# Performance work log

Measured on AMD Instinct MI355X. Metric: run time of the kernel, lower is better.

## Reference

```python
import jax, jax.numpy as jnp
import numpy as np

L = 3          # num_layer
D = 128        # emb_dim
N_INST = 40000
N_NET = 10000
N = N_INST + N_NET
E = 800000
EPS = 1e-5


def setup_inputs() -> dict:
    key = jax.random.key(0)
    ks = jax.random.split(key, 16)
    g = lambda k, shape: jax.random.normal(k, shape, jnp.float32) * 0.05
    return {
        'x': jax.random.normal(ks[0], (N_INST, 11), jnp.float32),
        'x_net': jax.random.normal(ks[1], (N_NET, 3), jnp.float32),
        # encoder for instance nodes: 11 -> 2D -> D
        'enc_W1': g(ks[2], (2 * D, 11)), 'enc_b1': jnp.zeros((2 * D,), jnp.float32),
        'enc_W2': g(ks[3], (D, 2 * D)), 'enc_b2': jnp.zeros((D,), jnp.float32),
        # encoder for net nodes: 3 -> D -> D
        'encn_W1': g(ks[4], (D, 3)), 'encn_b1': jnp.zeros((D,), jnp.float32),
        'encn_W2': g(ks[5], (D, D)), 'encn_b2': jnp.zeros((D,), jnp.float32),
        # forward-direction GCN convs
        'conv_W': g(ks[6], (L, D, D)), 'conv_b': jnp.zeros((L, D), jnp.float32),
        'conv_root': g(ks[7], (L, D)),
        # reverse-direction GCN convs
        'rconv_W': g(ks[8], (L, D, D)), 'rconv_b': jnp.zeros((L, D), jnp.float32),
        'rconv_root': g(ks[9], (L, D)),
        # layernorms
        'ln_g': jnp.ones((L, D), jnp.float32), 'ln_b': jnp.zeros((L, D), jnp.float32),
        # graph edge list
        'src': jax.random.randint(ks[10], (E,), 0, N, jnp.int32),
        'dst': jax.random.randint(ks[11], (E,), 0, N, jnp.int32),
        'num_instances': N_INST,
    }


def _lrelu(v):
    return jnp.where(v >= 0, v, 0.1 * v)


def _gcn_conv(h, W, b, root, e_src, e_dst, deg, dinv):
    # h: [N, D]; e_src/e_dst: [E]; deg/dinv: [N]
    x = h @ W.T + b                                   # [N, D]
    norm = dinv[e_src] * dinv[e_dst]                  # [E]
    msg = norm[:, None] * jax.nn.relu(x[e_src])       # [E, D] gather + scale
    agg = jax.ops.segment_sum(msg, e_dst, num_segments=N)  # [N, D] scatter-add
    self_loop = jax.nn.relu(x + root) / deg[:, None]
    return agg + self_loop


def reference(x, x_net, enc_W1, enc_b1, enc_W2, enc_b2,
              encn_W1, encn_b1, encn_W2, encn_b2,
              conv_W, conv_b, conv_root, rconv_W, rconv_b, rconv_root,
              ln_g, ln_b, src, dst, num_instances):
    # node encoders
    h_inst = _lrelu(_lrelu(x @ enc_W1.T + enc_b1) @ enc_W2.T + enc_b2)
    h_net = _lrelu(_lrelu(x_net @ encn_W1.T + encn_b1) @ encn_W2.T + encn_b2)
    h = jnp.concatenate([h_inst, h_net], axis=0)      # [N, D]

    ones = jnp.ones((E,), jnp.float32)
    deg_in = jax.ops.segment_sum(ones, dst, num_segments=N) + 1.0
    deg_out = jax.ops.segment_sum(ones, src, num_segments=N) + 1.0
    dinv_in = jnp.where(jnp.isinf(deg_in ** -0.5), 0.0, deg_in ** -0.5)
    dinv_out = jnp.where(jnp.isinf(deg_out ** -0.5), 0.0, deg_out ** -0.5)

    h_list = [h]
    for l in range(L):
        hf = _gcn_conv(h, conv_W[l], conv_b[l], conv_root[l], src, dst, deg_in, dinv_in)
        # reverse graph: edges flipped -> src/dst swapped, degrees swap roles
        hr = _gcn_conv(h, rconv_W[l], rconv_b[l], rconv_root[l], dst, src, deg_out, dinv_out)
        s = hf + hr
        mu = jnp.mean(s, axis=-1, keepdims=True)
        var = jnp.mean((s - mu) ** 2, axis=-1, keepdims=True)
        s = (s - mu) * jax.lax.rsqrt(var + EPS) * ln_g[l] + ln_b[l]
        s = _lrelu(s)
        h = s + h  # residual
        h_list.append(h)

    rep = jnp.concatenate(h_list, axis=1)             # [N, (L+1)*D] (JK='concat')
    return rep[num_instances:]                        # net-node representations
```

## Files before the change

kernel.cpp:

```cpp
#include <hip/hip_runtime.h>
#include <hip/hip_bf16.h>


constexpr int D = 128;
constexpr int CAP = 48;

typedef float f32x4 __attribute__((ext_vector_type(4)));
typedef float f32x2 __attribute__((ext_vector_type(2)));
typedef __bf16 bf16x8v __attribute__((ext_vector_type(8)));

#if defined(__has_builtin)
# if __has_builtin(__builtin_amdgcn_cvt_pk_f32_fp8) && __has_builtin(__builtin_amdgcn_cvt_pk_f32_fp8)
#  define HAS_HW_FP8 1
# endif
#endif
#ifndef HAS_HW_FP8
# define HAS_HW_FP8 0
#endif

__device__ __forceinline__ unsigned short f2bf(float f) {
    unsigned u = __float_as_uint(f);
    unsigned r = (u + 0x7fffu + ((u >> 16) & 1u)) >> 16;
    return (unsigned short)r;
}
__device__ __forceinline__ float bflo(unsigned u) { return __uint_as_float(u << 16); }
__device__ __forceinline__ float bfhi(unsigned u) { return __uint_as_float(u & 0xffff0000u); }

__device__ __forceinline__ unsigned enc_fp8_1(float f) {
    unsigned u = __float_as_uint(f);
    u += 0x7FFFFu + ((u >> 20) & 1u);
    int e = (int)(u >> 23) - 120;
    unsigned m = (u >> 20) & 7u;
    if (e <= 0) return 0u;
    if (e > 15 || (e == 15 && m == 7u)) return 0x7Eu;
    return ((unsigned)e << 3) | m;
}
__device__ __forceinline__ unsigned pack_fp8x2(float a, float b) {
#if HAS_HW_FP8
    return (unsigned)__builtin_amdgcn_cvt_pk_fp8_f32(a, b, 0, false) & 0xFFFFu;
#else
    return enc_fp8_1(a) | (enc_fp8_1(b) << 8);
#endif
}
__device__ __forceinline__ float dec_fp8_1(unsigned b) {
    unsigned e = (b >> 3) & 0xFu, m = b & 7u;
    unsigned bits = ((e + 120u) << 23) | (m << 20);
    return e ? __uint_as_float(bits) : 0.0f;
}
__device__ __forceinline__ void dec_fp8x4(unsigned u, float o[4]) {
#if HAS_HW_FP8
    f32x2 lo = __builtin_amdgcn_cvt_pk_f32_fp8((int)u, false);
    f32x2 hi = __builtin_amdgcn_cvt_pk_f32_fp8((int)u, true);
    o[0] = lo.x; o[1] = lo.y; o[2] = hi.x; o[3] = hi.y;
#else
    o[0] = dec_fp8_1(u & 0xFF); o[1] = dec_fp8_1((u >> 8) & 0xFF);
    o[2] = dec_fp8_1((u >> 16) & 0xFF); o[3] = dec_fp8_1(u >> 24);
#endif
}

__global__ __launch_bounds__(256) void fill_cast(
    const int* __restrict__ src, const int* __restrict__ dst, int E,
    int* __restrict__ cnt_i, int* __restrict__ cnt_o,
    unsigned short* __restrict__ slot_i, unsigned short* __restrict__ slot_o,
    int N, int prange, int chunk, int FB,
    const float* __restrict__ cW, const float* __restrict__ rW,
    const float* __restrict__ eW2, const float* __restrict__ enW2,
    unsigned short* __restrict__ cWb, unsigned short* __restrict__ rWb,
    unsigned short* __restrict__ eW2b, unsigned short* __restrict__ enW2b,
    int ncw, int nrw, int new2, int nenw2)
{
    if ((int)blockIdx.x >= FB) {
        int i = ((int)blockIdx.x - FB) * 256 + (int)threadIdx.x;
        if (i < ncw) { cWb[i] = f2bf(cW[i]); return; }
        i -= ncw;
        if (i < nrw) { rWb[i] = f2bf(rW[i]); return; }
        i -= nrw;
        if (i < new2) { eW2b[i] = f2bf(eW2[i]); return; }
        i -= new2;
        if (i < nenw2) enW2b[i] = f2bf(enW2[i]);
        return;
    }
    int part = blockIdx.x & 7;
    int slice = blockIdx.x >> 3;
    int lo = part * prange, hi = min(N, lo + prange);
    int e0 = slice * chunk, e1 = min(E, e0 + chunk);
    for (int e = e0 + (int)threadIdx.x * 8; e + 8 <= e1; e += 2048) {
        int4 s4a = *(const int4*)(src + e);
        int4 s4b = *(const int4*)(src + e + 4);
        int4 d4a = *(const int4*)(dst + e);
        int4 d4b = *(const int4*)(dst + e + 4);
        int ss[8] = {s4a.x, s4a.y, s4a.z, s4a.w, s4b.x, s4b.y, s4b.z, s4b.w};
        int dd[8] = {d4a.x, d4a.y, d4a.z, d4a.w, d4b.x, d4b.y, d4b.z, d4b.w};
        #pragma unroll
        for (int j = 0; j < 8; ++j) {
            int d = dd[j], s = ss[j];
            if (d >= lo && d < hi) {
                int p = atomicAdd(&cnt_i[d], 1);
                if (p < CAP) slot_i[(size_t)d * CAP + p] = (unsigned short)s;
            }
            if (s >= lo && s < hi) {
                int p = atomicAdd(&cnt_o[s], 1);
                if (p < CAP) slot_o[(size_t)s * CAP + p] = (unsigned short)d;
            }
        }
    }
}

__global__ __launch_bounds__(256) void enc_gemm1(
    const float* __restrict__ x, const float* __restrict__ x_net,
    const float* __restrict__ W1, const float* __restrict__ b1,
    const float* __restrict__ Wn1, const float* __restrict__ bn1,
    unsigned short* __restrict__ t1, unsigned short* __restrict__ t2,
    int NI, int NN, int nbi)
{
    int b = blockIdx.x;
    const float *A, *W, *bias; unsigned short* Cb;
    int M, K, OUT, ldc, bx, by;
    if (b < nbi * 4) {
        bx = b >> 2; by = b & 3;
        A = x; W = W1; bias = b1; Cb = t1; M = NI; K = 11; OUT = 256; ldc = 256;
    } else {
        b -= nbi * 4;
        bx = b >> 1; by = b & 1;
        A = x_net; W = Wn1; bias = bn1; Cb = t2; M = NN; K = 3; OUT = 128; ldc = 128;
    }
    __shared__ __align__(16) float As[16][68];
    __shared__ __align__(16) float Ws[16][68];
    int row0 = bx * 64, col0 = by * 64;
    int t = threadIdx.x;
    int tx = t & 15, ty = t >> 4;
    float acc[4][4] = {};
    {
        #pragma unroll
        for (int i = 0; i < 4; ++i) {
            int e = t + i * 256;
            int m = e >> 4, k = e & 15;
            int gr = row0 + m;
            As[k][m] = (gr < M && k < K) ? A[(size_t)gr * K + k] : 0.f;
            int gn = col0 + m;
            Ws[k][m] = (gn < OUT && k < K) ? W[(size_t)gn * K + k] : 0.f;
        }
        __syncthreads();
        #pragma unroll
        for (int k = 0; k < 16; ++k) {
            float4 av = *(const float4*)&As[k][ty * 4];
            float4 bv = *(const float4*)&Ws[k][tx * 4];
            float a[4] = {av.x, av.y, av.z, av.w};
            float bb[4] = {bv.x, bv.y, bv.z, bv.w};
            #pragma unroll
            for (int ii = 0; ii < 4; ++ii)
                #pragma unroll
                for (int jj = 0; jj < 4; ++jj)
                    acc[ii][jj] = fmaf(a[ii], bb[jj], acc[ii][jj]);
        }
    }
    #pragma unroll
    for (int ii = 0; ii < 4; ++ii) {
        int gr = row0 + ty * 4 + ii;
        if (gr >= M) continue;
        #pragma unroll
        for (int jj = 0; jj < 4; ++jj) {
            int gn = col0 + tx * 4 + jj;
            if (gn >= OUT) continue;
            float v = acc[ii][jj] + bias[gn];
            v = (v >= 0.f) ? v : 0.1f * v;
            Cb[(size_t)gr * ldc + gn] = f2bf(v);
        }
    }
}

__device__ __forceinline__ void mfma_core(
    const unsigned short* __restrict__ A, const unsigned short* __restrict__ W,
    int M, int K, int row0, int lane, f32x4 acc[8])
{
    int arc = min(row0 + (lane & 15), M - 1);
    int kq = (lane >> 4) * 8;
    const unsigned short* arow = A + (size_t)arc * K + kq;
    const unsigned short* wbase = W + (size_t)(lane & 15) * K + kq;
    for (int k0 = 0; k0 < K; k0 += 32) {
        bf16x8v a = *reinterpret_cast<const bf16x8v*>(arow + k0);
        #pragma unroll
        for (int j = 0; j < 8; ++j) {
            bf16x8v b = *reinterpret_cast<const bf16x8v*>(wbase + (size_t)j * 16 * K + k0);
            acc[j] = __builtin_amdgcn_mfma_f32_16x16x32_bf16(a, b, acc[j], 0, 0, 0);
        }
    }
}

__global__ __launch_bounds__(256) void enc_gemm2(
    const unsigned short* __restrict__ t1, const unsigned short* __restrict__ t2,
    const unsigned short* __restrict__ W2b, const unsigned short* __restrict__ Wn2b,
    const float* __restrict__ b2, const float* __restrict__ bn2,
    float* __restrict__ h, unsigned short* __restrict__ hb,
    float* __restrict__ out, int NI, int NN, int nbi)
{
    int b = blockIdx.x;
    const unsigned short *A, *W; const float* bias;
    int M, K; bool isnet;
    int wave = threadIdx.x >> 6;
    int lane = threadIdx.x & 63;
    int row0;
    if (b < nbi) {
        A = t1; W = W2b; bias = b2; M = NI; K = 256; isnet = false;
        row0 = b * 64 + wave * 16;
    } else {
        A = t2; W = Wn2b; bias = bn2; M = NN; K = 128; isnet = true;
        row0 = (b - nbi) * 64 + wave * 16;
    }
    f32x4 acc[8];
    #pragma unroll
    for (int j = 0; j < 8; ++j) acc[j] = (f32x4){0.f, 0.f, 0.f, 0.f};
    mfma_core(A, W, M, K, row0, lane, acc);
    int cbase = lane & 15;
    int rsub = (lane >> 4) * 4;
    #pragma unroll
    for (int j = 0; j < 8; ++j) {
        int f = j * 16 + cbase;
        float bv = bias[f];
        #pragma unroll
        for (int q = 0; q < 4; ++q) {
            int r = row0 + rsub + q;
            if (r >= M) continue;
            float v = acc[j][q] + bv;
            v = (v >= 0.f) ? v : 0.1f * v;
            int gr = isnet ? NI + r : r;
            h[(size_t)gr * D + f] = v;
            hb[(size_t)gr * D + f] = f2bf(v);
            if (isnet) out[(size_t)r * 512 + f] = v;
        }
    }
}

__global__ __launch_bounds__(256) void conv_gemm(
    const unsigned short* __restrict__ hb,
    const unsigned short* __restrict__ Wf, const unsigned short* __restrict__ Wr,
    const float* __restrict__ biasf, const float* __restrict__ biasr,
    const float* __restrict__ rootf, const float* __restrict__ rootr,
    const int* __restrict__ cnt_i, const int* __restrict__ cnt_o,
    unsigned char* __restrict__ mf, unsigned char* __restrict__ mr,
    unsigned short* __restrict__ sl, int M)
{
    int wave = threadIdx.x >> 6;
    int lane = threadIdx.x & 63;
    int row0 = blockIdx.x * 64 + wave * 16;
    f32x4 accf[8], accr[8];
    #pragma unroll
    for (int j = 0; j < 8; ++j) {
        accf[j] = (f32x4){0.f, 0.f, 0.f, 0.f};
        accr[j] = (f32x4){0.f, 0.f, 0.f, 0.f};
    }
    int arc = min(row0 + (lane & 15), M - 1);
    int kq = (lane >> 4) * 8;
    const unsigned short* arow = hb + (size_t)arc * D + kq;
    const unsigned short* wfb = Wf + (size_t)(lane & 15) * D + kq;
    const unsigned short* wrb = Wr + (size_t)(lane & 15) * D + kq;
    for (int k0 = 0; k0 < D; k0 += 32) {
        bf16x8v a = *reinterpret_cast<const bf16x8v*>(arow + k0);
        #pragma unroll
        for (int j = 0; j < 8; ++j) {
            bf16x8v bf_ = *reinterpret_cast<const bf16x8v*>(wfb + (size_t)j * 16 * D + k0);
            accf[j] = __builtin_amdgcn_mfma_f32_16x16x32_bf16(a, bf_, accf[j], 0, 0, 0);
        }
        #pragma unroll
        for (int j = 0; j < 8; ++j) {
            bf16x8v br_ = *reinterpret_cast<const bf16x8v*>(wrb + (size_t)j * 16 * D + k0);
            accr[j] = __builtin_amdgcn_mfma_f32_16x16x32_bf16(a, br_, accr[j], 0, 0, 0);
        }
    }
    int cbase = lane & 15;
    int rsub = (lane >> 4) * 4;
    float di[4], dou[4], rdi[4], rdo[4];
    #pragma unroll
    for (int q = 0; q < 4; ++q) {
        int r = min(row0 + rsub + q, M - 1);
        float ci = (float)cnt_i[r] + 1.0f;
        float co = (float)cnt_o[r] + 1.0f;
        di[q] = rsqrtf(ci) * 64.0f; rdi[q] = 1.0f / ci;
        dou[q] = rsqrtf(co) * 64.0f; rdo[q] = 1.0f / co;
    }
    #pragma unroll
    for (int j = 0; j < 8; j += 2) {
        int f0 = j * 16 + cbase, f1 = f0 + 16;
        float bf0 = biasf[f0], bf1 = biasf[f1];
        float br0 = biasr[f0], br1 = biasr[f1];
        float rf0 = rootf[f0], rf1 = rootf[f1];
        float rr0 = rootr[f0], rr1 = rootr[f1];
        #pragma unroll
        for (int q = 0; q < 4; ++q) {
            int r = row0 + rsub + q;
            if (r >= M) continue;
            float vf0 = accf[j][q] + bf0, vf1 = accf[j + 1][q] + bf1;
            float vr0 = accr[j][q] + br0, vr1 = accr[j + 1][q] + br1;
            size_t o0 = (size_t)r * D + f0, o1 = (size_t)r * D + f1;
            unsigned em = pack_fp8x2(di[q] * fmaxf(vf0, 0.f), di[q] * fmaxf(vf1, 0.f));
            mf[o0] = (unsigned char)(em & 0xFF);
            mf[o1] = (unsigned char)(em >> 8);
            unsigned er = pack_fp8x2(dou[q] * fmaxf(vr0, 0.f), dou[q] * fmaxf(vr1, 0.f));
            mr[o0] = (unsigned char)(er & 0xFF);
            mr[o1] = (unsigned char)(er >> 8);
            sl[o0] = f2bf(fmaxf(vf0 + rf0, 0.f) * rdi[q] + fmaxf(vr0 + rr0, 0.f) * rdo[q]);
            sl[o1] = f2bf(fmaxf(vf1 + rf1, 0.f) * rdi[q] + fmaxf(vr1 + rr1, 0.f) * rdo[q]);
        }
    }
}

__device__ __forceinline__ void gather_tail(
    const unsigned char* __restrict__ m, int idx, int k, int sn,
    int rl, size_t fb, float a[4])
{
    for (; k + 8 <= sn; k += 8) {
        int p0 = __shfl(idx, k + rl);
        int p1 = __shfl(idx, k + 2 + rl);
        int p2 = __shfl(idx, k + 4 + rl);
        int p3 = __shfl(idx, k + 6 + rl);
        unsigned u0 = *(const unsigned*)(m + (((size_t)p0) << 7) + fb);
        unsigned u1 = *(const unsigned*)(m + (((size_t)p1) << 7) + fb);
        unsigned u2 = *(const unsigned*)(m + (((size_t)p2) << 7) + fb);
        unsigned u3 = *(const unsigned*)(m + (((size_t)p3) << 7) + fb);
        float t0[4], t1_[4], t2_[4], t3[4];
        dec_fp8x4(u0, t0); dec_fp8x4(u1, t1_); dec_fp8x4(u2, t2_); dec_fp8x4(u3, t3);
        a[0] += t0[0] + t1_[0] + t2_[0] + t3[0];
        a[1] += t0[1] + t1_[1] + t2_[1] + t3[1];
        a[2] += t0[2] + t1_[2] + t2_[2] + t3[2];
        a[3] += t0[3] + t1_[3] + t2_[3] + t3[3];
    }
    for (; k + 2 <= sn; k += 2) {
        int p = __shfl(idx, k + rl);
        unsigned u = *(const unsigned*)(m + (((size_t)p) << 7) + fb);
        float t[4];
        dec_fp8x4(u, t);
        a[0] += t[0]; a[1] += t[1]; a[2] += t[2]; a[3] += t[3];
    }
    if (k < sn) {
        int p = __shfl(idx, k);
        if (rl == 0) {
            unsigned u = *(const unsigned*)(m + (((size_t)p) << 7) + fb);
            float t[4];
            dec_fp8x4(u, t);
            a[0] += t[0]; a[1] += t[1]; a[2] += t[2]; a[3] += t[3];
        }
    }
}

__global__ __launch_bounds__(256) void agg_kernel(
    const unsigned char* __restrict__ mf, const unsigned char* __restrict__ mr,
    const unsigned short* __restrict__ sl,
    float* __restrict__ h, unsigned short* __restrict__ hb,
    const int* __restrict__ cnt_i, const unsigned short* __restrict__ slot_i,
    const int* __restrict__ cnt_o, const unsigned short* __restrict__ slot_o,
    const float* __restrict__ g, const float* __restrict__ bta,
    float* __restrict__ out, int N, int NI, int layer)
{
    int wid = (blockIdx.x * blockDim.x + threadIdx.x) >> 6;
    if (wid >= N) return;
    int lane = threadIdx.x & 63;
    int fl = lane & 31;
    int rl = lane >> 5;
    size_t fb = (size_t)fl * 4;

    int ci_raw = cnt_i[wid], co_raw = cnt_o[wid];
    int sni = min(ci_raw, CAP), sno = min(co_raw, CAP);
    float degi = (float)ci_raw + 1.0f, dego = (float)co_raw + 1.0f;

    int idxA = (lane < sni) ? (int)slot_i[(size_t)wid * CAP + lane] : 0;
    int idxB = (lane < sno) ? (int)slot_o[(size_t)wid * CAP + lane] : 0;

    float a[4] = {0.f, 0.f, 0.f, 0.f};
    float b[4] = {0.f, 0.f, 0.f, 0.f};
    int k = 0;
    while (k + 8 <= sni && k + 8 <= sno) {
        int pA0 = __shfl(idxA, k + rl);
        int pA1 = __shfl(idxA, k + 2 + rl);
        int pA2 = __shfl(idxA, k + 4 + rl);
        int pA3 = __shfl(idxA, k + 6 + rl);
        int pB0 = __shfl(idxB, k + rl);
        int pB1 = __shfl(idxB, k + 2 + rl);
        int pB2 = __shfl(idxB, k + 4 + rl);
        int pB3 = __shfl(idxB, k + 6 + rl);
        unsigned uA0 = *(const unsigned*)(mf + (((size_t)pA0) << 7) + fb);
        unsigned uA1 = *(const unsigned*)(mf + (((size_t)pA1) << 7) + fb);
        unsigned uA2 = *(const unsigned*)(mf + (((size_t)pA2) << 7) + fb);
        unsigned uA3 = *(const unsigned*)(mf + (((size_t)pA3) << 7) + fb);
        unsigned uB0 = *(const unsigned*)(mr + (((size_t)pB0) << 7) + fb);
        unsigned uB1 = *(const unsigned*)(mr + (((size_t)pB1) << 7) + fb);
        unsigned uB2 = *(const unsigned*)(mr + (((size_t)pB2) << 7) + fb);
        unsigned uB3 = *(const unsigned*)(mr + (((size_t)pB3) << 7) + fb);
        float tA0[4], tA1[4], tA2[4], tA3[4], tB0[4], tB1[4], tB2[4], tB3[4];
        dec_fp8x4(uA0, tA0); dec_fp8x4(uA1, tA1); dec_fp8x4(uA2, tA2); dec_fp8x4(uA3, tA3);
        dec_fp8x4(uB0, tB0); dec_fp8x4(uB1, tB1); dec_fp8x4(uB2, tB2); dec_fp8x4(uB3, tB3);
        #pragma unroll
        for (int j = 0; j < 4; ++j) {
            a[j] += tA0[j] + tA1[j] + tA2[j] + tA3[j];
            b[j] += tB0[j] + tB1[j] + tB2[j] + tB3[j];
        }
        k += 8;
    }
    gather_tail(mf, idxA, k, sni, rl, fb, a);
    gather_tail(mr, idxB, k, sno, rl, fb, b);

    #pragma unroll
    for (int j = 0; j < 4; ++j) {
        a[j] += __shfl_xor(a[j], 32);
        b[j] += __shfl_xor(b[j], 32);
    }
    int half = lane >> 1;
    float ta0 = __shfl(a[0], half), ta1 = __shfl(a[1], half);
    float ta2 = __shfl(a[2], half), ta3 = __shfl(a[3], half);
    float tb0 = __shfl(b[0], half), tb1 = __shfl(b[1], half);
    float tb2 = __shfl(b[2], half), tb3 = __shfl(b[3], half);
    float ga0 = (lane & 1) ? ta2 : ta0;
    float ga1 = (lane & 1) ? ta3 : ta1;
    float gb0 = (lane & 1) ? tb2 : tb0;
    float gb1 = (lane & 1) ? tb3 : tb1;

    int d0 = lane * 2;
    float di = rsqrtf(degi) * 0.015625f;
    float dou = rsqrtf(dego) * 0.015625f;
    unsigned usl = *(const unsigned*)(sl + (((size_t)wid) << 7) + d0);
    float s_0 = di * ga0 + dou * gb0 + bflo(usl);
    float s_1 = di * ga1 + dou * gb1 + bfhi(usl);

    float sm = s_0 + s_1;
    float sq = s_0 * s_0 + s_1 * s_1;
    #pragma unroll
    for (int o = 32; o >= 1; o >>= 1) {
        sm += __shfl_xor(sm, o);
        sq += __shfl_xor(sq, o);
    }
    float mu = sm * (1.0f / 128.0f);
    float var = sq * (1.0f / 128.0f) - mu * mu;
    float rs = rsqrtf(var + 1e-5f);

    float2 gv = *(const float2*)(g + d0);
    float2 bv = *(const float2*)(bta + d0);
    float2 hv = *(const float2*)(h + (((size_t)wid) << 7) + d0);
    float y0 = (s_0 - mu) * rs * gv.x + bv.x;
    float y1 = (s_1 - mu) * rs * gv.y + bv.y;
    y0 = (y0 >= 0.f) ? y0 : 0.1f * y0;
    y1 = (y1 >= 0.f) ? y1 : 0.1f * y1;
    y0 += hv.x; y1 += hv.y;
    *(float2*)(h + (((size_t)wid) << 7) + d0) = make_float2(y0, y1);
    if (layer < 2) {
        unsigned packed = (unsigned)f2bf(y0) | ((unsigned)f2bf(y1) << 16);
        *(unsigned*)(hb + (((size_t)wid) << 7) + d0) = packed;
    }
    if (wid >= NI) {
        *(float2*)(out + (size_t)(wid - NI) * 512 + (size_t)(layer + 1) * 128 + d0) = make_float2(y0, y1);
    }
}

static inline int cdiv(int a, int b) { return (a + b - 1) / b; }

extern "C" void kernel_launch(void* const* d_in, const int* in_sizes, int n_in,
                              void* d_out, int out_size, void* d_ws, size_t ws_size,
                              hipStream_t stream)
{
    const float* x        = (const float*)d_in[0];
    const float* x_net    = (const float*)d_in[1];
    const float* enc_W1   = (const float*)d_in[2];
    const float* enc_b1   = (const float*)d_in[3];
    const float* enc_W2   = (const float*)d_in[4];
    const float* enc_b2   = (const float*)d_in[5];
    const float* encn_W1  = (const float*)d_in[6];
    const float* encn_b1  = (const float*)d_in[7];
    const float* encn_W2  = (const float*)d_in[8];
    const float* encn_b2  = (const float*)d_in[9];
    const float* conv_W   = (const float*)d_in[10];
    const float* conv_b   = (const float*)d_in[11];
    const float* conv_root= (const float*)d_in[12];
    const float* rconv_W  = (const float*)d_in[13];
    const float* rconv_b  = (const float*)d_in[14];
    const float* rconv_root=(const float*)d_in[15];
    const float* ln_g     = (const float*)d_in[16];
    const float* ln_b     = (const float*)d_in[17];
    const int*   src      = (const int*)d_in[18];
    const int*   dst      = (const int*)d_in[19];

    const int NI = in_sizes[0] / 11;
    const int NN = in_sizes[1] / 3;
    const int N  = NI + NN;
    const int E  = in_sizes[18];
    float* out = (float*)d_out;

    char* ws = (char*)d_ws;
    size_t offq = 0;
    auto alloc = [&](size_t bytes) -> void* {
        void* p = ws + offq;
        offq += (bytes + 255) & ~(size_t)255;
        return p;
    };
    float*          h    = (float*)alloc((size_t)N * D * 4);
    unsigned short* hb   = (unsigned short*)alloc((size_t)N * D * 2);
    unsigned char*  mf   = (unsigned char*)alloc((size_t)N * D);
    unsigned char*  mr   = (unsigned char*)alloc((size_t)N * D);
    unsigned short* sl   = (unsigned short*)alloc((size_t)N * D * 2);
    unsigned short* tmp2b = (unsigned short*)alloc((size_t)NN * D * 2);
    unsigned short* slot_i = (unsigned short*)alloc((size_t)N * CAP * 2);
    unsigned short* slot_o = (unsigned short*)alloc((size_t)N * CAP * 2);
    int*   cnt    = (int*)alloc((size_t)2 * N * 4);
    int*   cnt_i  = cnt;
    int*   cnt_o  = cnt + N;
    unsigned short* encW2b  = (unsigned short*)alloc((size_t)in_sizes[4] * 2);
    unsigned short* encnW2b = (unsigned short*)alloc((size_t)in_sizes[8] * 2);
    unsigned short* convWb  = (unsigned short*)alloc((size_t)in_sizes[10] * 2);
    unsigned short* rconvWb = (unsigned short*)alloc((size_t)in_sizes[13] * 2);
    unsigned short* tmp1b = (unsigned short*)mf;

    const int ncw = in_sizes[10], nrw = in_sizes[13];
    const int new2 = in_sizes[4], nenw2 = in_sizes[8];

    hipMemsetAsync(cnt, 0, (size_t)2 * N * 4, stream);

    const int prange = cdiv(N, 8);
    const int chunk = 8192;
    const int NS = cdiv(E, chunk);
    const int FB = 8 * NS;
    const int CB = cdiv(ncw + nrw + new2 + nenw2, 256);
    fill_cast<<<FB + CB, 256, 0, stream>>>(
        src, dst, E, cnt_i, cnt_o, slot_i, slot_o, N, prange, chunk, FB,
        conv_W, rconv_W, enc_W2, encn_W2, convWb, rconvWb, encW2b, encnW2b,
        ncw, nrw, new2, nenw2);

    const int nbi1 = cdiv(NI, 64);
    const int nbn1 = cdiv(NN, 64);
    enc_gemm1<<<nbi1 * 4 + nbn1 * 2, 256, 0, stream>>>(
        x, x_net, enc_W1, enc_b1, encn_W1, encn_b1, tmp1b, tmp2b, NI, NN, nbi1);
    enc_gemm2<<<nbi1 + nbn1, 256, 0, stream>>>(
        tmp1b, tmp2b, encW2b, encnW2b, enc_b2, encn_b2, h, hb, out, NI, NN, nbi1);

    for (int l = 0; l < 3; ++l) {
        conv_gemm<<<cdiv(N, 64), 256, 0, stream>>>(
            hb, convWb + (size_t)l * D * D, rconvWb + (size_t)l * D * D,
            conv_b + (size_t)l * D, rconv_b + (size_t)l * D,
            conv_root + (size_t)l * D, rconv_root + (size_t)l * D,
            cnt_i, cnt_o, mf, mr, sl, N);
        agg_kernel<<<cdiv(N * 64, 256), 256, 0, stream>>>(
            mf, mr, sl, h, hb, cnt_i, slot_i, cnt_o, slot_o,
            ln_g + (size_t)l * D, ln_b + (size_t)l * D,
            out, N, NI, l);
    }
}
```

Measured before the change: 410.4 us.

## Fuse encoder GEMM1 into fill kernel, pad slot stride, use nontemporal accesses

Merges the first encoder GEMM into the adjacency-fill/weight-cast kernel as extra blocks, removing one launch and letting the encoder work overlap the atomic-heavy edge bucketing. Pads the per-node slot rows from 48 to 64 entries so each row is 128-byte aligned. Switches streaming loads and stores of edges, slots, h and the output to nontemporal builtins to reduce cache pollution. This costs more slot memory, and the nontemporal hints may hurt if h is reread while still in cache. It also fixes the FP8 builtin detection check so it tests both intrinsics.

```diff
diff --git a/kernel.cpp b/kernel.cpp
--- a/kernel.cpp
+++ b/kernel.cpp
@@ -4,13 +4,15 @@
 
 constexpr int D = 128;
 constexpr int CAP = 48;
+constexpr int SSTR = 64;
 
 typedef float f32x4 __attribute__((ext_vector_type(4)));
 typedef float f32x2 __attribute__((ext_vector_type(2)));
+typedef int   i32x4 __attribute__((ext_vector_type(4)));
 typedef __bf16 bf16x8v __attribute__((ext_vector_type(8)));
 
 #if defined(__has_builtin)
-# if __has_builtin(__builtin_amdgcn_cvt_pk_f32_fp8) && __has_builtin(__builtin_amdgcn_cvt_pk_f32_fp8)
+# if __has_builtin(__builtin_amdgcn_cvt_pk_f32_fp8) && __has_builtin(__builtin_amdgcn_cvt_pk_fp8_f32)
 #  define HAS_HW_FP8 1
 # endif
 #endif
@@ -58,18 +60,50 @@
 #endif
 }
 
-__global__ __launch_bounds__(256) void fill_cast(
+__global__ __launch_bounds__(256) void fill_cast_enc1(
     const int* __restrict__ src, const int* __restrict__ dst, int E,
     int* __restrict__ cnt_i, int* __restrict__ cnt_o,
     unsigned short* __restrict__ slot_i, unsigned short* __restrict__ slot_o,
-    int N, int prange, int chunk, int FB,
+    int N, int prange, int chunk, int FB, int CB,
     const float* __restrict__ cW, const float* __restrict__ rW,
     const float* __restrict__ eW2, const float* __restrict__ enW2,
     unsigned short* __restrict__ cWb, unsigned short* __restrict__ rWb,
     unsigned short* __restrict__ eW2b, unsigned short* __restrict__ enW2b,
-    int ncw, int nrw, int new2, int nenw2)
-{
-    if ((int)blockIdx.x >= FB) {
+    int ncw, int nrw, int new2, int nenw2,
+    const float* __restrict__ x, const float* __restrict__ x_net,
+    const float* __restrict__ W1, const float* __restrict__ b1,
+    const float* __restrict__ Wn1, const float* __restrict__ bn1,
+    unsigned short* __restrict__ t1, unsigned short* __restrict__ t2,
+    int NI, int NN, int nbi)
+{
+    if ((int)blockIdx.x < FB) {
+        int part = blockIdx.x & 7;
+        int slice = blockIdx.x >> 3;
+        int lo = part * prange, hi = min(N, lo + prange);
+        int e0 = slice * chunk, e1 = min(E, e0 + chunk);
+        for (int e = e0 + (int)threadIdx.x * 8; e + 8 <= e1; e += 2048) {
+            i32x4 s4a = __builtin_nontemporal_load((const i32x4*)(src + e));
+            i32x4 s4b = __builtin_nontemporal_load((const i32x4*)(src + e + 4));
+            i32x4 d4a = __builtin_nontemporal_load((const i32x4*)(dst + e));
+            i32x4 d4b = __builtin_nontemporal_load((const i32x4*)(dst + e + 4));
+            int ss[8] = {s4a.x, s4a.y, s4a.z, s4a.w, s4b.x, s4b.y, s4b.z, s4b.w};
+            int dd[8] = {d4a.x, d4a.y, d4a.z, d4a.w, d4b.x, d4b.y, d4b.z, d4b.w};
+            #pragma unroll
+            for (int j = 0; j < 8; ++j) {
+                int d = dd[j], s = ss[j];
+                if (d >= lo && d < hi) {
+                    int p = atomicAdd(&cnt_i[d], 1);
+                    if (p < CAP) slot_i[(size_t)d * SSTR + p] = (unsigned short)s;
+                }
+                if (s >= lo && s < hi) {
+                    int p = atomicAdd(&cnt_o[s], 1);
+                    if (p < CAP) slot_o[(size_t)s * SSTR + p] = (unsigned short)d;
+                }
+            }
+        }
+        return;
+    }
+    if ((int)blockIdx.x < FB + CB) {
         int i = ((int)blockIdx.x - FB) * 256 + (int)threadIdx.x;
         if (i < ncw) { cWb[i] = f2bf(cW[i]); return; }
         i -= ncw;
@@ -80,40 +114,7 @@
         if (i < nenw2) enW2b[i] = f2bf(enW2[i]);
         return;
     }
-    int part = blockIdx.x & 7;
-    int slice = blockIdx.x >> 3;
-    int lo = part * prange, hi = min(N, lo + prange);
-    int e0 = slice * chunk, e1 = min(E, e0 + chunk);
-    for (int e = e0 + (int)threadIdx.x * 8; e + 8 <= e1; e += 2048) {
-        int4 s4a = *(const int4*)(src + e);
-        int4 s4b = *(const int4*)(src + e + 4);
-        int4 d4a = *(const int4*)(dst + e);
-        int4 d4b = *(const int4*)(dst + e + 4);
-        int ss[8] = {s4a.x, s4a.y, s4a.z, s4a.w, s4b.x, s4b.y, s4b.z, s4b.w};
-        int dd[8] = {d4a.x, d4a.y, d4a.z, d4a.w, d4b.x, d4b.y, d4b.z, d4b.w};
-        #pragma unroll
-        for (int j = 0; j < 8; ++j) {
-            int d = dd[j], s = ss[j];
-            if (d >= lo && d < hi) {
-                int p = atomicAdd(&cnt_i[d], 1);
-                if (p < CAP) slot_i[(size_t)d * CAP + p] = (unsigned short)s;
-            }
-            if (s >= lo && s < hi) {
-                int p = atomicAdd(&cnt_o[s], 1);
-                if (p < CAP) slot_o[(size_t)s * CAP + p] = (unsigned short)d;
-            }
-        }
-    }
-}
-
-__global__ __launch_bounds__(256) void enc_gemm1(
-    const float* __restrict__ x, const float* __restrict__ x_net,
-    const float* __restrict__ W1, const float* __restrict__ b1,
-    const float* __restrict__ Wn1, const float* __restrict__ bn1,
-    unsigned short* __restrict__ t1, unsigned short* __restrict__ t2,
-    int NI, int NN, int nbi)
-{
-    int b = blockIdx.x;
+    int b = (int)blockIdx.x - FB - CB;
     const float *A, *W, *bias; unsigned short* Cb;
     int M, K, OUT, ldc, bx, by;
     if (b < nbi * 4) {
@@ -130,29 +131,27 @@
     int t = threadIdx.x;
     int tx = t & 15, ty = t >> 4;
     float acc[4][4] = {};
-    {
-        #pragma unroll
-        for (int i = 0; i < 4; ++i) {
-            int e = t + i * 256;
-            int m = e >> 4, k = e & 15;
-            int gr = row0 + m;
-            As[k][m] = (gr < M && k < K) ? A[(size_t)gr * K + k] : 0.f;
-            int gn = col0 + m;
-            Ws[k][m] = (gn < OUT && k < K) ? W[(size_t)gn * K + k] : 0.f;
-        }
-        __syncthreads();
-        #pragma unroll
-        for (int k = 0; k < 16; ++k) {
-            float4 av = *(const float4*)&As[k][ty * 4];
-            float4 bv = *(const float4*)&Ws[k][tx * 4];
-            float a[4] = {av.x, av.y, av.z, av.w};
-            float bb[4] = {bv.x, bv.y, bv.z, bv.w};
+    #pragma unroll
+    for (int i = 0; i < 4; ++i) {
+        int e = t + i * 256;
+        int m = e >> 4, k = e & 15;
+        int gr = row0 + m;
+        As[k][m] = (gr < M && k < K) ? A[(size_t)gr * K + k] : 0.f;
+        int gn = col0 + m;
+        Ws[k][m] = (gn < OUT && k < K) ? W[(size_t)gn * K + k] : 0.f;
+    }
+    __syncthreads();
+    #pragma unroll
+    for (int k = 0; k < 16; ++k) {
+        float4 av = *(const float4*)&As[k][ty * 4];
+        float4 bv = *(const float4*)&Ws[k][tx * 4];
+        float a[4] = {av.x, av.y, av.z, av.w};
+        float bb[4] = {bv.x, bv.y, bv.z, bv.w};
+        #pragma unroll
+        for (int ii = 0; ii < 4; ++ii)
             #pragma unroll
-            for (int ii = 0; ii < 4; ++ii)
-                #pragma unroll
-                for (int jj = 0; jj < 4; ++jj)
-                    acc[ii][jj] = fmaf(a[ii], bb[jj], acc[ii][jj]);
-        }
+            for (int jj = 0; jj < 4; ++jj)
+                acc[ii][jj] = fmaf(a[ii], bb[jj], acc[ii][jj]);
     }
     #pragma unroll
     for (int ii = 0; ii < 4; ++ii) {
@@ -362,8 +361,10 @@
     int sni = min(ci_raw, CAP), sno = min(co_raw, CAP);
     float degi = (float)ci_raw + 1.0f, dego = (float)co_raw + 1.0f;
 
-    int idxA = (lane < sni) ? (int)slot_i[(size_t)wid * CAP + lane] : 0;
-    int idxB = (lane < sno) ? (int)slot_o[(size_t)wid * CAP + lane] : 0;
+    int idxA = (lane < sni)
+        ? (int)__builtin_nontemporal_load(slot_i + (size_t)wid * SSTR + lane) : 0;
+    int idxB = (lane < sno)
+        ? (int)__builtin_nontemporal_load(slot_o + (size_t)wid * SSTR + lane) : 0;
 
     float a[4] = {0.f, 0.f, 0.f, 0.f};
     float b[4] = {0.f, 0.f, 0.f, 0.f};
@@ -416,7 +417,7 @@
     int d0 = lane * 2;
     float di = rsqrtf(degi) * 0.015625f;
     float dou = rsqrtf(dego) * 0.015625f;
-    unsigned usl = *(const unsigned*)(sl + (((size_t)wid) << 7) + d0);
+    unsigned usl = __builtin_nontemporal_load((const unsigned*)(sl + (((size_t)wid) << 7) + d0));
     float s_0 = di * ga0 + dou * gb0 + bflo(usl);
     float s_1 = di * ga1 + dou * gb1 + bfhi(usl);
 
@@ -433,19 +434,21 @@
 
     float2 gv = *(const float2*)(g + d0);
     float2 bv = *(const float2*)(bta + d0);
-    float2 hv = *(const float2*)(h + (((size_t)wid) << 7) + d0);
+    f32x2 hv = __builtin_nontemporal_load((const f32x2*)(h + (((size_t)wid) << 7) + d0));
     float y0 = (s_0 - mu) * rs * gv.x + bv.x;
     float y1 = (s_1 - mu) * rs * gv.y + bv.y;
     y0 = (y0 >= 0.f) ? y0 : 0.1f * y0;
     y1 = (y1 >= 0.f) ? y1 : 0.1f * y1;
     y0 += hv.x; y1 += hv.y;
-    *(float2*)(h + (((size_t)wid) << 7) + d0) = make_float2(y0, y1);
+    f32x2 res; res.x = y0; res.y = y1;
+    __builtin_nontemporal_store(res, (f32x2*)(h + (((size_t)wid) << 7) + d0));
     if (layer < 2) {
         unsigned packed = (unsigned)f2bf(y0) | ((unsigned)f2bf(y1) << 16);
         *(unsigned*)(hb + (((size_t)wid) << 7) + d0) = packed;
     }
     if (wid >= NI) {
-        *(float2*)(out + (size_t)(wid - NI) * 512 + (size_t)(layer + 1) * 128 + d0) = make_float2(y0, y1);
+        __builtin_nontemporal_store(res,
+            (f32x2*)(out + (size_t)(wid - NI) * 512 + (size_t)(layer + 1) * 128 + d0));
     }
 }
 
@@ -495,8 +498,8 @@
     unsigned char*  mr   = (unsigned char*)alloc((size_t)N * D);
     unsigned short* sl   = (unsigned short*)alloc((size_t)N * D * 2);
     unsigned short* tmp2b = (unsigned short*)alloc((size_t)NN * D * 2);
-    unsigned short* slot_i = (unsigned short*)alloc((size_t)N * CAP * 2);
-    unsigned short* slot_o = (unsigned short*)alloc((size_t)N * CAP * 2);
+    unsigned short* slot_i = (unsigned short*)alloc((size_t)N * SSTR * 2);
+    unsigned short* slot_o = (unsigned short*)alloc((size_t)N * SSTR * 2);
     int*   cnt    = (int*)alloc((size_t)2 * N * 4);
     int*   cnt_i  = cnt;
     int*   cnt_o  = cnt + N;
@@ -509,22 +512,22 @@
     const int ncw = in_sizes[10], nrw = in_sizes[13];
     const int new2 = in_sizes[4], nenw2 = in_sizes[8];
 
-    hipMemsetAsync(cnt, 0, (size_t)2 * N * 4, stream);
+    (void)hipMemsetAsync(cnt, 0, (size_t)2 * N * 4, stream);
 
     const int prange = cdiv(N, 8);
     const int chunk = 8192;
     const int NS = cdiv(E, chunk);
     const int FB = 8 * NS;
     const int CB = cdiv(ncw + nrw + new2 + nenw2, 256);
-    fill_cast<<<FB + CB, 256, 0, stream>>>(
-        src, dst, E, cnt_i, cnt_o, slot_i, slot_o, N, prange, chunk, FB,
-        conv_W, rconv_W, enc_W2, encn_W2, convWb, rconvWb, encW2b, encnW2b,
-        ncw, nrw, new2, nenw2);
-
     const int nbi1 = cdiv(NI, 64);
     const int nbn1 = cdiv(NN, 64);
-    enc_gemm1<<<nbi1 * 4 + nbn1 * 2, 256, 0, stream>>>(
+    const int EB1 = nbi1 * 4 + nbn1 * 2;
+    fill_cast_enc1<<<FB + CB + EB1, 256, 0, stream>>>(
+        src, dst, E, cnt_i, cnt_o, slot_i, slot_o, N, prange, chunk, FB, CB,
+        conv_W, rconv_W, enc_W2, encn_W2, convWb, rconvWb, encW2b, encnW2b,
+        ncw, nrw, new2, nenw2,
         x, x_net, enc_W1, enc_b1, encn_W1, encn_b1, tmp1b, tmp2b, NI, NN, nbi1);
+
     enc_gemm2<<<nbi1 + nbn1, 256, 0, stream>>>(
         tmp1b, tmp2b, encW2b, encnW2b, enc_b2, encn_b2, h, hb, out, NI, NN, nbi1);
 
```

Result: slower. 448.4 us (+9.3%).

## Fuse the two encoder GEMM stages into one kernel via shared-memory intermediate

Applied to the files above, without the earlier changes.

Merges the encoder's first FP32 GEMM and its second MFMA bf16 GEMM into a single kernel. The hidden activation tile (64 rows by up to 256 columns of bf16) stays in LDS instead of going through a global temporary buffer. This removes one kernel launch and the global write and read of the intermediate. In exchange each block holds about 34KB of LDS, which may lower occupancy, and the first stage now runs serially over column tiles inside one block. The FP8 builtin detection check is also corrected, which may switch the hardware FP8 path on.

```diff
diff --git a/kernel.cpp b/kernel.cpp
--- a/kernel.cpp
+++ b/kernel.cpp
@@ -10,7 +10,7 @@
 typedef __bf16 bf16x8v __attribute__((ext_vector_type(8)));
 
 #if defined(__has_builtin)
-# if __has_builtin(__builtin_amdgcn_cvt_pk_f32_fp8) && __has_builtin(__builtin_amdgcn_cvt_pk_f32_fp8)
+# if __has_builtin(__builtin_amdgcn_cvt_pk_f32_fp8) && __has_builtin(__builtin_amdgcn_cvt_pk_fp8_f32)
 #  define HAS_HW_FP8 1
 # endif
 #endif
@@ -106,41 +106,47 @@
     }
 }
 
-__global__ __launch_bounds__(256) void enc_gemm1(
+__global__ __launch_bounds__(256) void enc_fused(
     const float* __restrict__ x, const float* __restrict__ x_net,
     const float* __restrict__ W1, const float* __restrict__ b1,
     const float* __restrict__ Wn1, const float* __restrict__ bn1,
-    unsigned short* __restrict__ t1, unsigned short* __restrict__ t2,
-    int NI, int NN, int nbi)
+    const unsigned short* __restrict__ W2b, const unsigned short* __restrict__ Wn2b,
+    const float* __restrict__ b2, const float* __restrict__ bn2,
+    float* __restrict__ h, unsigned short* __restrict__ hb,
+    float* __restrict__ out, int NI, int NN, int nbi)
 {
-    int b = blockIdx.x;
-    const float *A, *W, *bias; unsigned short* Cb;
-    int M, K, OUT, ldc, bx, by;
-    if (b < nbi * 4) {
-        bx = b >> 2; by = b & 3;
-        A = x; W = W1; bias = b1; Cb = t1; M = NI; K = 11; OUT = 256; ldc = 256;
-    } else {
-        b -= nbi * 4;
-        bx = b >> 1; by = b & 1;
-        A = x_net; W = Wn1; bias = bn1; Cb = t2; M = NN; K = 3; OUT = 128; ldc = 128;
-    }
+    __shared__ __align__(16) unsigned short T[64][264];
     __shared__ __align__(16) float As[16][68];
     __shared__ __align__(16) float Ws[16][68];
-    int row0 = bx * 64, col0 = by * 64;
+
+    int b = blockIdx.x;
+    bool isnet = b >= nbi;
+    const float* A   = isnet ? x_net : x;
+    const float* Wl1 = isnet ? Wn1 : W1;
+    const float* bl1 = isnet ? bn1 : b1;
+    const unsigned short* Wl2 = isnet ? Wn2b : W2b;
+    const float* bl2 = isnet ? bn2 : b2;
+    const int M   = isnet ? NN : NI;
+    const int K1  = isnet ? 3 : 11;
+    const int OUT = isnet ? 128 : 256;
+    const int row0 = (isnet ? b - nbi : b) * 64;
+
     int t = threadIdx.x;
     int tx = t & 15, ty = t >> 4;
-    float acc[4][4] = {};
-    {
+
+    for (int col0 = 0; col0 < OUT; col0 += 64) {
+        __syncthreads();
         #pragma unroll
         for (int i = 0; i < 4; ++i) {
             int e = t + i * 256;
             int m = e >> 4, k = e & 15;
             int gr = row0 + m;
-            As[k][m] = (gr < M && k < K) ? A[(size_t)gr * K + k] : 0.f;
+            As[k][m] = (gr < M && k < K1) ? A[(size_t)gr * K1 + k] : 0.f;
             int gn = col0 + m;
-            Ws[k][m] = (gn < OUT && k < K) ? W[(size_t)gn * K + k] : 0.f;
+            Ws[k][m] = (k < K1) ? Wl1[(size_t)gn * K1 + k] : 0.f;
         }
         __syncthreads();
+        float acc[4][4] = {};
         #pragma unroll
         for (int k = 0; k < 16; ++k) {
             float4 av = *(const float4*)&As[k][ty * 4];
@@ -153,75 +159,48 @@
                 for (int jj = 0; jj < 4; ++jj)
                     acc[ii][jj] = fmaf(a[ii], bb[jj], acc[ii][jj]);
         }
-    }
-    #pragma unroll
-    for (int ii = 0; ii < 4; ++ii) {
-        int gr = row0 + ty * 4 + ii;
-        if (gr >= M) continue;
-        #pragma unroll
-        for (int jj = 0; jj < 4; ++jj) {
-            int gn = col0 + tx * 4 + jj;
-            if (gn >= OUT) continue;
-            float v = acc[ii][jj] + bias[gn];
-            v = (v >= 0.f) ? v : 0.1f * v;
-            Cb[(size_t)gr * ldc + gn] = f2bf(v);
-        }
-    }
-}
-
-__device__ __forceinline__ void mfma_core(
-    const unsigned short* __restrict__ A, const unsigned short* __restrict__ W,
-    int M, int K, int row0, int lane, f32x4 acc[8])
-{
-    int arc = min(row0 + (lane & 15), M - 1);
+        #pragma unroll
+        for (int ii = 0; ii < 4; ++ii) {
+            int lr = ty * 4 + ii;
+            #pragma unroll
+            for (int jj = 0; jj < 4; ++jj) {
+                int c = col0 + tx * 4 + jj;
+                float v = acc[ii][jj] + bl1[c];
+                v = (v >= 0.f) ? v : 0.1f * v;
+                T[lr][c] = f2bf(v);
+            }
+        }
+    }
+    __syncthreads();
+
+    int wave = t >> 6, lane = t & 63;
+    int lrow0 = wave * 16;
+    int K2 = OUT;
+    f32x4 acc2[8];
+    #pragma unroll
+    for (int j = 0; j < 8; ++j) acc2[j] = (f32x4){0.f, 0.f, 0.f, 0.f};
     int kq = (lane >> 4) * 8;
-    const unsigned short* arow = A + (size_t)arc * K + kq;
-    const unsigned short* wbase = W + (size_t)(lane & 15) * K + kq;
-    for (int k0 = 0; k0 < K; k0 += 32) {
+    const unsigned short* arow = &T[lrow0 + (lane & 15)][kq];
+    const unsigned short* wbase = Wl2 + (size_t)(lane & 15) * K2 + kq;
+    for (int k0 = 0; k0 < K2; k0 += 32) {
         bf16x8v a = *reinterpret_cast<const bf16x8v*>(arow + k0);
         #pragma unroll
         for (int j = 0; j < 8; ++j) {
-            bf16x8v b = *reinterpret_cast<const bf16x8v*>(wbase + (size_t)j * 16 * K + k0);
-            acc[j] = __builtin_amdgcn_mfma_f32_16x16x32_bf16(a, b, acc[j], 0, 0, 0);
-        }
-    }
-}
-
-__global__ __launch_bounds__(256) void enc_gemm2(
-    const unsigned short* __restrict__ t1, const unsigned short* __restrict__ t2,
-    const unsigned short* __restrict__ W2b, const unsigned short* __restrict__ Wn2b,
-    const float* __restrict__ b2, const float* __restrict__ bn2,
-    float* __restrict__ h, unsigned short* __restrict__ hb,
-    float* __restrict__ out, int NI, int NN, int nbi)
-{
-    int b = blockIdx.x;
-    const unsigned short *A, *W; const float* bias;
-    int M, K; bool isnet;
-    int wave = threadIdx.x >> 6;
-    int lane = threadIdx.x & 63;
-    int row0;
-    if (b < nbi) {
-        A = t1; W = W2b; bias = b2; M = NI; K = 256; isnet = false;
-        row0 = b * 64 + wave * 16;
-    } else {
-        A = t2; W = Wn2b; bias = bn2; M = NN; K = 128; isnet = true;
-        row0 = (b - nbi) * 64 + wave * 16;
-    }
-    f32x4 acc[8];
-    #pragma unroll
-    for (int j = 0; j < 8; ++j) acc[j] = (f32x4){0.f, 0.f, 0.f, 0.f};
-    mfma_core(A, W, M, K, row0, lane, acc);
+            bf16x8v bb = *reinterpret_cast<const bf16x8v*>(wbase + (size_t)j * 16 * K2 + k0);
+            acc2[j] = __builtin_amdgcn_mfma_f32_16x16x32_bf16(a, bb, acc2[j], 0, 0, 0);
+        }
+    }
     int cbase = lane & 15;
     int rsub = (lane >> 4) * 4;
     #pragma unroll
     for (int j = 0; j < 8; ++j) {
         int f = j * 16 + cbase;
-        float bv = bias[f];
+        float bv = bl2[f];
         #pragma unroll
         for (int q = 0; q < 4; ++q) {
-            int r = row0 + rsub + q;
+            int r = row0 + lrow0 + rsub + q;
             if (r >= M) continue;
-            float v = acc[j][q] + bv;
+            float v = acc2[j][q] + bv;
             v = (v >= 0.f) ? v : 0.1f * v;
             int gr = isnet ? NI + r : r;
             h[(size_t)gr * D + f] = v;
@@ -494,7 +473,6 @@
     unsigned char*  mf   = (unsigned char*)alloc((size_t)N * D);
     unsigned char*  mr   = (unsigned char*)alloc((size_t)N * D);
     unsigned short* sl   = (unsigned short*)alloc((size_t)N * D * 2);
-    unsigned short* tmp2b = (unsigned short*)alloc((size_t)NN * D * 2);
     unsigned short* slot_i = (unsigned short*)alloc((size_t)N * CAP * 2);
     unsigned short* slot_o = (unsigned short*)alloc((size_t)N * CAP * 2);
     int*   cnt    = (int*)alloc((size_t)2 * N * 4);
@@ -504,12 +482,11 @@
     unsigned short* encnW2b = (unsigned short*)alloc((size_t)in_sizes[8] * 2);
     unsigned short* convWb  = (unsigned short*)alloc((size_t)in_sizes[10] * 2);
     unsigned short* rconvWb = (unsigned short*)alloc((size_t)in_sizes[13] * 2);
-    unsigned short* tmp1b = (unsigned short*)mf;
 
     const int ncw = in_sizes[10], nrw = in_sizes[13];
     const int new2 = in_sizes[4], nenw2 = in_sizes[8];
 
-    hipMemsetAsync(cnt, 0, (size_t)2 * N * 4, stream);
+    (void)hipMemsetAsync(cnt, 0, (size_t)2 * N * 4, stream);
 
     const int prange = cdiv(N, 8);
     const int chunk = 8192;
@@ -523,10 +500,9 @@
 
     const int nbi1 = cdiv(NI, 64);
     const int nbn1 = cdiv(NN, 64);
-    enc_gemm1<<<nbi1 * 4 + nbn1 * 2, 256, 0, stream>>>(
-        x, x_net, enc_W1, enc_b1, encn_W1, encn_b1, tmp1b, tmp2b, NI, NN, nbi1);
-    enc_gemm2<<<nbi1 + nbn1, 256, 0, stream>>>(
-        tmp1b, tmp2b, encW2b, encnW2b, enc_b2, encn_b2, h, hb, out, NI, NN, nbi1);
+    enc_fused<<<nbi1 + nbn1, 256, 0, stream>>>(
+        x, x_net, enc_W1, enc_b1, encn_W1, encn_b1, encW2b, encnW2b,
+        enc_b2, encn_b2, h, hb, out, NI, NN, nbi1);
 
     for (int l = 0; l < 3; ++l) {
         conv_gemm<<<cdiv(N, 64), 256, 0, stream>>>(
```

After: 399.8 us. -2.6%, faster.
